# Performance work log

Measured on AMD Instinct MI355X. Metric: run time of the kernel, lower is better.

The kernel has to match this reference:

```python
import jax, jax.numpy as jnp
import numpy as np


def setup_inputs() -> dict:
    key = jax.random.key(0)
    k1, k2, k3, k4, k5 = jax.random.split(key, 5)
    N, T, D, H = 64, 512, 512, 512
    std = 1.0 / np.sqrt(H)
    return {
        "x": jax.random.normal(k1, (N, T, D), dtype=jnp.float32),
        "weight_xh": jax.random.uniform(k2, (D, 4 * H), jnp.float32, -std, std),
        "weight_hh": jax.random.uniform(k3, (H, 4 * H), jnp.float32, -std, std),
        "bias_xh": jax.random.uniform(k4, (4 * H,), jnp.float32, -std, std),
        "bias_hh": jax.random.uniform(k5, (4 * H,), jnp.float32, -std, std),
    }


def reference(x, weight_xh, weight_hh, bias_xh, bias_hh):
    # x: (N, T, D) -> (T, N, D)
    x = jnp.transpose(x, (1, 0, 2))
    T, N, _ = x.shape
    H = weight_hh.shape[0]
    # Input projection for all timesteps at once: (T, N, 4H)
    xh = jnp.einsum("tnd,dk->tnk", x, weight_xh) + bias_xh

    def step(carry, xh_t):
        h_prev, c_prev = carry
        gates = xh_t + h_prev @ weight_hh + bias_hh  # (N, 4H)
        i = jax.nn.sigmoid(gates[:, 0:H])
        f = jax.nn.sigmoid(gates[:, H:2 * H])
        g = jnp.tanh(gates[:, 2 * H:3 * H])
        o = jax.nn.sigmoid(gates[:, 3 * H:4 * H])
        c = f * c_prev + i * g
        h = o * jnp.tanh(c)
        return (h, c), h

    h0 = jnp.zeros((N, H), dtype=x.dtype)
    c0 = jnp.zeros((N, H), dtype=x.dtype)
    _, y = jax.lax.scan(step, (h0, c0), xh)  # y: (T, N, H)
    return jnp.transpose(y, (1, 0, 2))  # (N, T, H)
```

## Files before the change

### kernel.cpp

```cpp
#include <hip/hip_runtime.h>

typedef unsigned short u16;
typedef unsigned int   u32;
typedef unsigned long long u64;
typedef __attribute__((ext_vector_type(8))) short short8;
typedef __attribute__((ext_vector_type(4))) float f32x4;
typedef __attribute__((ext_vector_type(2))) unsigned long long u64x2;

#define NB   64
#define TS   512
#define HD   512
#define RG   4
#define CG   32
#define NBLK (RG*CG)
#define HP   130

__device__ __forceinline__ u16 f2bf(float x) {
    union { float f; u32 i; } v; v.f = x;
    u32 r = (v.i + 0x7fffu + ((v.i >> 16) & 1u)) >> 16;
    return (u16)r;
}
__device__ __forceinline__ u32 pack2bf(float a, float b) {
    return (u32)f2bf(a) | ((u32)f2bf(b) << 16);
}
__device__ __forceinline__ float sigmf(float x) { return 1.0f / (1.0f + __expf(-x)); }
__device__ __forceinline__ float tanhf_fast(float x) { return 1.0f - 2.0f / (__expf(2.0f * x) + 1.0f); }

__global__ void cvt_x_k(const float* __restrict__ in, u16* __restrict__ out, int n) {
    int i = (blockIdx.x * blockDim.x + threadIdx.x) * 8;
    const int stride = gridDim.x * blockDim.x * 8;
    for (; i < n; i += stride) {
        const f32x4 a = *(const f32x4*)(in + i);
        const f32x4 b = *(const f32x4*)(in + i + 4);
        u32 q[4];
        q[0] = pack2bf(a[0], a[1]);
        q[1] = pack2bf(a[2], a[3]);
        q[2] = pack2bf(b[0], b[1]);
        q[3] = pack2bf(b[2], b[3]);
        *(f32x4*)(out + i) = *(f32x4*)q;
    }
}

__global__ void transpose_cvt_k(const float* __restrict__ in, u16* __restrict__ out,
                                int R, int C) {
    __shared__ float tile[32][33];
    const int c0 = blockIdx.x * 32;
    const int r0 = blockIdx.y * 32;
    const int tx = threadIdx.x & 31;
    const int ty = threadIdx.x >> 5;
#pragma unroll
    for (int i = 0; i < 32; i += 8)
        tile[ty + i][tx] = in[(size_t)(r0 + ty + i) * C + c0 + tx];
    __syncthreads();
#pragma unroll
    for (int i = 0; i < 32; i += 8)
        out[(size_t)(c0 + ty + i) * R + r0 + tx] = f2bf(tile[tx][ty + i]);
}

__global__ __launch_bounds__(256, 1) void lstm_fused(
    const u16*   __restrict__ xbg,
    const u16*   __restrict__ WtX,
    const u16*   __restrict__ WtH,
    const float* __restrict__ bxh,
    const float* __restrict__ bhh,
    u64*   __restrict__ hbuf,
    float* __restrict__ y,
    u32*   __restrict__ flags)
{
    const int bid  = blockIdx.x;
    const int r    = bid & 3;
    const int cg   = bid >> 2;
    const int tid  = threadIdx.x;
    const int lane = tid & 63;
    const int wv   = tid >> 6;
    const int m15  = lane & 15;
    const int kq   = lane >> 4;
    const int n0   = r * 16;
    const int gcol0 = wv * 512 + cg * 16;

    __shared__ u64   ldsH[16 * HP];
    __shared__ float gbuf[4][16][17];
    __shared__ u16   ht[16][16];

    short8 wx[16], wh[16];
    {
        const u16* px = WtX + (size_t)(gcol0 + m15) * 512 + kq * 8;
        const u16* ph = WtH + (size_t)(gcol0 + m15) * 512 + kq * 8;
#pragma unroll
        for (int kc = 0; kc < 16; ++kc) {
            wx[kc] = *(const short8*)(px + kc * 32);
            wh[kc] = *(const short8*)(ph + kc * 32);
        }
    }
    const float bsum = bxh[gcol0 + m15] + bhh[gcol0 + m15];

    const int erow = tid >> 4;
    const int ecol = tid & 15;
    const int en   = n0 + erow;
    const int hcol = cg * 16 + ecol;
    float cst = 0.0f;

    const int lrow = 4 * wv + (lane >> 4);
    const int c0   = (lane & 15) * 8;

    short8 xb[16];
    {
        const u16* xg = xbg + ((size_t)(n0 + m15) * TS + 0) * HD + kq * 8;
#pragma unroll
        for (int kc = 0; kc < 16; ++kc)
            xb[kc] = *(const short8*)(xg + kc * 32);
    }

    for (int t = 0; t < TS; ++t) {
        u64 hq[8];
        if (t > 0) {
            const u32* fl = flags + (size_t)(t - 1) * (RG * CG) + r * CG;
            u32 v;
            do {
                v = __hip_atomic_load(fl + (lane & 31), __ATOMIC_RELAXED,
                                      __HIP_MEMORY_SCOPE_AGENT);
            } while (!__all(v != 0u));

            const u64* gsrc = hbuf + (size_t)((t - 1) & 3) * (NB * 128)
                            + (size_t)(n0 + lrow) * 128 + c0;
#pragma unroll
            for (int i = 0; i < 8; ++i)
                hq[i] = __hip_atomic_load(gsrc + i, __ATOMIC_RELAXED,
                                          __HIP_MEMORY_SCOPE_AGENT);
        }

        f32x4 a0 = {0.f,0.f,0.f,0.f}, a1 = {0.f,0.f,0.f,0.f};
        f32x4 a2 = {0.f,0.f,0.f,0.f}, a3 = {0.f,0.f,0.f,0.f};
#pragma unroll
        for (int kc = 0; kc < 4; ++kc) {
            a0 = __builtin_amdgcn_mfma_f32_16x16x32_bf16(xb[4*kc + 0], wx[4*kc + 0], a0, 0, 0, 0);
            a1 = __builtin_amdgcn_mfma_f32_16x16x32_bf16(xb[4*kc + 1], wx[4*kc + 1], a1, 0, 0, 0);
            a2 = __builtin_amdgcn_mfma_f32_16x16x32_bf16(xb[4*kc + 2], wx[4*kc + 2], a2, 0, 0, 0);
            a3 = __builtin_amdgcn_mfma_f32_16x16x32_bf16(xb[4*kc + 3], wx[4*kc + 3], a3, 0, 0, 0);
        }

        if (t > 0) {
            u64* ldst = &ldsH[lrow * HP + c0];
            *(u64x2*)(ldst)     = (u64x2){hq[0], hq[1]};
            *(u64x2*)(ldst + 2) = (u64x2){hq[2], hq[3]};
            *(u64x2*)(ldst + 4) = (u64x2){hq[4], hq[5]};
            *(u64x2*)(ldst + 6) = (u64x2){hq[6], hq[7]};
            __syncthreads();

            const u16* lh = (const u16*)ldsH + m15 * (HP * 4) + kq * 8;
#pragma unroll
            for (int kc = 0; kc < 4; ++kc) {
                short8 h0 = *(const short8*)(lh + (4*kc + 0) * 32);
                short8 h1 = *(const short8*)(lh + (4*kc + 1) * 32);
                short8 h2 = *(const short8*)(lh + (4*kc + 2) * 32);
                short8 h3 = *(const short8*)(lh + (4*kc + 3) * 32);
                a0 = __builtin_amdgcn_mfma_f32_16x16x32_bf16(h0, wh[4*kc + 0], a0, 0, 0, 0);
                a1 = __builtin_amdgcn_mfma_f32_16x16x32_bf16(h1, wh[4*kc + 1], a1, 0, 0, 0);
                a2 = __builtin_amdgcn_mfma_f32_16x16x32_bf16(h2, wh[4*kc + 2], a2, 0, 0, 0);
                a3 = __builtin_amdgcn_mfma_f32_16x16x32_bf16(h3, wh[4*kc + 3], a3, 0, 0, 0);
            }
        }

        {
            f32x4 g4 = a0 + a1 + a2 + a3;
#pragma unroll
            for (int j = 0; j < 4; ++j)
                gbuf[wv][kq * 4 + j][m15] = g4[j] + bsum;
        }
        __syncthreads();

        {
            const float gi = gbuf[0][erow][ecol];
            const float gf = gbuf[1][erow][ecol];
            const float gg = gbuf[2][erow][ecol];
            const float go = gbuf[3][erow][ecol];
            const float iv = sigmf(gi);
            const float fv = sigmf(gf);
            const float gv = tanhf_fast(gg);
            const float ov = sigmf(go);
            cst = fv * cst + iv * gv;
            const float hv = ov * tanhf_fast(cst);
            y[((size_t)en * 512 + t) * 512 + hcol] = hv;
            ht[erow][ecol] = f2bf(hv);
        }
        __syncthreads();

        if (tid < 64) {
            const int row = tid >> 2;
            const int c4  = tid & 3;
            const u64 v = *(const u64*)&ht[row][c4 * 4];
            __hip_atomic_store(hbuf + (size_t)(t & 3) * (NB * 128)
                               + (size_t)(n0 + row) * 128 + cg * 4 + c4, v,
                               __ATOMIC_RELAXED, __HIP_MEMORY_SCOPE_AGENT);
        }
        __syncthreads();

        if (t < TS - 1 && tid == 0) {
            __hip_atomic_store(flags + (size_t)t * (RG * CG) + r * CG + cg, 1u,
                               __ATOMIC_RELAXED, __HIP_MEMORY_SCOPE_AGENT);
        }

        if (t + 1 < TS) {
            const u16* xg = xbg + ((size_t)(n0 + m15) * TS + (t + 1)) * HD + kq * 8;
#pragma unroll
            for (int kc = 0; kc < 16; ++kc)
                xb[kc] = *(const short8*)(xg + kc * 32);
        }
    }
}

extern "C" void kernel_launch(void* const* d_in, const int* in_sizes, int n_in,
                              void* d_out, int out_size, void* d_ws, size_t ws_size,
                              hipStream_t stream) {
    const float* x   = (const float*)d_in[0];
    const float* wxh = (const float*)d_in[1];
    const float* whh = (const float*)d_in[2];
    const float* bxh = (const float*)d_in[3];
    const float* bhh = (const float*)d_in[4];
    float* y = (float*)d_out;

    char* ws = (char*)d_ws;
    u32* flags = (u32*)ws;
    u64* hbuf  = (u64*)(ws + (size_t)(1 << 18));
    u16* WtX   = (u16*)(ws + (size_t)(2 << 18));
    u16* WtH   = (u16*)(ws + (size_t)(2 << 18) + (size_t)2048 * 512 * 2);
    u16* xbg   = (u16*)(ws + (size_t)(2 << 18) + (size_t)2 * 2048 * 512 * 2);

    (void)hipMemsetAsync(flags, 0, (size_t)TS * RG * CG * sizeof(u32), stream);

    cvt_x_k<<<2048, 256, 0, stream>>>(x, xbg, NB * TS * HD);

    dim3 tgrid(2048 / 32, 512 / 32);
    transpose_cvt_k<<<tgrid, 256, 0, stream>>>(wxh, WtX, 512, 2048);
    transpose_cvt_k<<<tgrid, 256, 0, stream>>>(whh, WtH, 512, 2048);

    lstm_fused<<<dim3(NBLK), dim3(256), 0, stream>>>(xbg, WtX, WtH, bxh, bhh,
                                                     hbuf, y, flags);
}
```

Before: 2.143 ms.

## Replace flag-based step sync with timestep-tagged hidden-state words

Each hidden-state value is now written as a 32-bit word: the bf16 value in the low half and the timestep tag in the high half. Consumers poll the data itself until every tag matches, then repack the values into LDS. This removes the separate flag array and its memset, the staging of h through shared memory, and two block barriers plus the extra flag round-trip on every recurrent step. In exchange the h exchange buffer is twice as large, and polling re-reads the whole data slice on each retry. Correctness also relies on stale tags in the reused 4-slot ring never matching the expected tag.

```diff
diff --git a/kernel.cpp b/kernel.cpp
--- a/kernel.cpp
+++ b/kernel.cpp
@@ -5,7 +5,7 @@
 typedef unsigned long long u64;
 typedef __attribute__((ext_vector_type(8))) short short8;
 typedef __attribute__((ext_vector_type(4))) float f32x4;
-typedef __attribute__((ext_vector_type(2))) unsigned long long u64x2;
+typedef __attribute__((ext_vector_type(4))) u32   u32x4;
 
 #define NB   64
 #define TS   512
@@ -13,7 +13,7 @@
 #define RG   4
 #define CG   32
 #define NBLK (RG*CG)
-#define HP   130
+#define LP   520
 
 __device__ __forceinline__ u16 f2bf(float x) {
     union { float f; u32 i; } v; v.f = x;
@@ -63,9 +63,8 @@
     const u16*   __restrict__ WtH,
     const float* __restrict__ bxh,
     const float* __restrict__ bhh,
-    u64*   __restrict__ hbuf,
-    float* __restrict__ y,
-    u32*   __restrict__ flags)
+    u32*   __restrict__ hbuf,
+    float* __restrict__ y)
 {
     const int bid  = blockIdx.x;
     const int r    = bid & 3;
@@ -78,9 +77,8 @@
     const int n0   = r * 16;
     const int gcol0 = wv * 512 + cg * 16;
 
-    __shared__ u64   ldsH[16 * HP];
+    __shared__ u16   ldsH[16 * LP];
     __shared__ float gbuf[4][16][17];
-    __shared__ u16   ht[16][16];
 
     short8 wx[16], wh[16];
     {
@@ -101,7 +99,7 @@
     float cst = 0.0f;
 
     const int lrow = 4 * wv + (lane >> 4);
-    const int c0   = (lane & 15) * 8;
+    const int c0   = (lane & 15) * 32;
 
     short8 xb[16];
     {
@@ -112,23 +110,6 @@
     }
 
     for (int t = 0; t < TS; ++t) {
-        u64 hq[8];
-        if (t > 0) {
-            const u32* fl = flags + (size_t)(t - 1) * (RG * CG) + r * CG;
-            u32 v;
-            do {
-                v = __hip_atomic_load(fl + (lane & 31), __ATOMIC_RELAXED,
-                                      __HIP_MEMORY_SCOPE_AGENT);
-            } while (!__all(v != 0u));
-
-            const u64* gsrc = hbuf + (size_t)((t - 1) & 3) * (NB * 128)
-                            + (size_t)(n0 + lrow) * 128 + c0;
-#pragma unroll
-            for (int i = 0; i < 8; ++i)
-                hq[i] = __hip_atomic_load(gsrc + i, __ATOMIC_RELAXED,
-                                          __HIP_MEMORY_SCOPE_AGENT);
-        }
-
         f32x4 a0 = {0.f,0.f,0.f,0.f}, a1 = {0.f,0.f,0.f,0.f};
         f32x4 a2 = {0.f,0.f,0.f,0.f}, a3 = {0.f,0.f,0.f,0.f};
 #pragma unroll
@@ -140,14 +121,38 @@
         }
 
         if (t > 0) {
-            u64* ldst = &ldsH[lrow * HP + c0];
-            *(u64x2*)(ldst)     = (u64x2){hq[0], hq[1]};
-            *(u64x2*)(ldst + 2) = (u64x2){hq[2], hq[3]};
-            *(u64x2*)(ldst + 4) = (u64x2){hq[4], hq[5]};
-            *(u64x2*)(ldst + 6) = (u64x2){hq[6], hq[7]};
+            const u32 tagexp = (u32)t;
+            const u64 pat  = ((u64)tagexp << 48) | ((u64)tagexp << 16);
+            const u64* src = (const u64*)(hbuf + (size_t)((t - 1) & 3) * (NB * HD)
+                                        + (size_t)(n0 + lrow) * HD + c0);
+            u64 hq[16];
+            bool ok;
+            do {
+#pragma unroll
+                for (int i = 0; i < 16; ++i)
+                    hq[i] = __hip_atomic_load(src + i, __ATOMIC_RELAXED,
+                                              __HIP_MEMORY_SCOPE_AGENT);
+                ok = true;
+#pragma unroll
+                for (int i = 0; i < 16; ++i)
+                    ok = ok && ((hq[i] & 0xFFFF0000FFFF0000ULL) == pat);
+            } while (!__all(ok));
+
+            u32 pk[16];
+#pragma unroll
+            for (int i = 0; i < 16; ++i) {
+                const u32 lo = (u32)hq[i];
+                const u32 hi = (u32)(hq[i] >> 32);
+                pk[i] = (lo & 0xFFFFu) | (hi << 16);
+            }
+            u32* ldst = (u32*)(ldsH + lrow * LP + (lane & 15) * 32);
+            *(u32x4*)(ldst)      = *(u32x4*)(pk);
+            *(u32x4*)(ldst + 4)  = *(u32x4*)(pk + 4);
+            *(u32x4*)(ldst + 8)  = *(u32x4*)(pk + 8);
+            *(u32x4*)(ldst + 12) = *(u32x4*)(pk + 12);
             __syncthreads();
 
-            const u16* lh = (const u16*)ldsH + m15 * (HP * 4) + kq * 8;
+            const u16* lh = ldsH + m15 * LP + kq * 8;
 #pragma unroll
             for (int kc = 0; kc < 4; ++kc) {
                 short8 h0 = *(const short8*)(lh + (4*kc + 0) * 32);
@@ -180,24 +185,11 @@
             const float ov = sigmf(go);
             cst = fv * cst + iv * gv;
             const float hv = ov * tanhf_fast(cst);
+            const u32 word = ((u32)(t + 1) << 16) | (u32)f2bf(hv);
+            __hip_atomic_store(hbuf + (size_t)(t & 3) * (NB * HD)
+                               + (size_t)en * HD + hcol, word,
+                               __ATOMIC_RELAXED, __HIP_MEMORY_SCOPE_AGENT);
             y[((size_t)en * 512 + t) * 512 + hcol] = hv;
-            ht[erow][ecol] = f2bf(hv);
-        }
-        __syncthreads();
-
-        if (tid < 64) {
-            const int row = tid >> 2;
-            const int c4  = tid & 3;
-            const u64 v = *(const u64*)&ht[row][c4 * 4];
-            __hip_atomic_store(hbuf + (size_t)(t & 3) * (NB * 128)
-                               + (size_t)(n0 + row) * 128 + cg * 4 + c4, v,
-                               __ATOMIC_RELAXED, __HIP_MEMORY_SCOPE_AGENT);
-        }
-        __syncthreads();
-
-        if (t < TS - 1 && tid == 0) {
-            __hip_atomic_store(flags + (size_t)t * (RG * CG) + r * CG + cg, 1u,
-                               __ATOMIC_RELAXED, __HIP_MEMORY_SCOPE_AGENT);
         }
 
         if (t + 1 < TS) {
@@ -220,13 +212,11 @@
     float* y = (float*)d_out;
 
     char* ws = (char*)d_ws;
-    u32* flags = (u32*)ws;
-    u64* hbuf  = (u64*)(ws + (size_t)(1 << 18));
-    u16* WtX   = (u16*)(ws + (size_t)(2 << 18));
-    u16* WtH   = (u16*)(ws + (size_t)(2 << 18) + (size_t)2048 * 512 * 2);
-    u16* xbg   = (u16*)(ws + (size_t)(2 << 18) + (size_t)2 * 2048 * 512 * 2);
-
-    (void)hipMemsetAsync(flags, 0, (size_t)TS * RG * CG * sizeof(u32), stream);
+    u32* hbuf = (u32*)ws;
+    u16* WtX  = (u16*)(ws + (size_t)(1 << 19));
+    u16* WtH  = (u16*)(ws + (size_t)(1 << 19) + (size_t)2048 * 512 * 2);
+    u16* xbg  = (u16*)(ws + (size_t)(1 << 19) + (size_t)2 * 2048 * 512 * 2);
+
 
     cvt_x_k<<<2048, 256, 0, stream>>>(x, xbg, NB * TS * HD);
 
@@ -235,5 +225,5 @@
     transpose_cvt_k<<<tgrid, 256, 0, stream>>>(whh, WtH, 512, 2048);
 
     lstm_fused<<<dim3(NBLK), dim3(256), 0, stream>>>(xbg, WtX, WtH, bxh, bhh,
-                                                     hbuf, y, flags);
-}
+                                                     hbuf, y);
+}
```

Result: slower. 2.737 ms (+27.7%).
